# Kernel tuning notes

Measured on AMD Instinct MI355X. Metric: run time of the kernel, lower is better.

## Reference

```python
import jax, jax.numpy as jnp
import numpy as np

N_NODES = 20000
N_EDGES = 320000
HEADS = 16
NEG_SLOPE = 0.2


def _gat_conv(x, src, dst, W, a_src, a_dst, b, heads, out_ch):
    # x: [N, F_in]; src/dst: [E'] (self-loops already appended)
    N = x.shape[0]
    h = (x @ W).reshape(N, heads, out_ch)                  # [N, H, C]
    alpha_s = jnp.sum(h * a_src, axis=-1)                  # [N, H]
    alpha_d = jnp.sum(h * a_dst, axis=-1)                  # [N, H]
    e = jax.nn.leaky_relu(alpha_s[src] + alpha_d[dst], NEG_SLOPE)  # [E', H]
    # segment softmax over edges grouped by destination node
    m = jax.ops.segment_max(e, dst, num_segments=N)        # [N, H]
    ex = jnp.exp(e - m[dst])
    denom = jax.ops.segment_sum(ex, dst, num_segments=N)
    alpha = ex / (denom[dst] + 1e-16)                      # [E', H]
    msg = h[src] * alpha[:, :, None]                       # [E', H, C]
    out = jax.ops.segment_sum(msg, dst, num_segments=N)    # [N, H, C]
    return out.reshape(N, heads * out_ch) + b


def _forward(x, edge_index, params):
    N = x.shape[0]
    loops = jnp.arange(N, dtype=edge_index.dtype)
    src = jnp.concatenate([edge_index[0], loops])
    dst = jnp.concatenate([edge_index[1], loops])
    for i, (W, a_s, a_d, b, out_ch) in enumerate(params):
        x = _gat_conv(x, src, dst, W, a_s, a_d, b, HEADS, out_ch)
        if i < len(params) - 1:
            x = jax.nn.relu(x)
    return jnp.sum(x, axis=0, keepdims=True)               # [1, 768]


def setup_inputs() -> dict:
    key = jax.random.key(0)
    ks = jax.random.split(key, 32)
    hid, heads, out_c = 64, HEADS, 3
    dims = [(3, hid), (hid * heads, hid), (hid * heads, hid), (hid * heads, hid), (hid * heads, hid), (hid * heads, out_c * heads)]
    inp = {}
    inp["x"] = jax.random.normal(ks[0], (N_NODES, 3), dtype=jnp.float32)
    inp["edge_index"] = jax.random.randint(ks[1], (2, N_EDGES), 0, N_NODES, dtype=jnp.int64)
    k = 2
    for li, (fin, c) in enumerate(dims, start=1):
        inp[f"W{li}"] = jax.random.normal(ks[k], (fin, heads * c), dtype=jnp.float32) * 0.1; k += 1
        inp[f"a{li}s"] = jax.random.normal(ks[k], (heads, c), dtype=jnp.float32) * 0.1; k += 1
        inp[f"a{li}d"] = jax.random.normal(ks[k], (heads, c), dtype=jnp.float32) * 0.1; k += 1
        inp[f"b{li}"] = jnp.zeros((heads * c,), dtype=jnp.float32)
    return inp


def reference(x, edge_index, W1, a1s, a1d, b1, W2, a2s, a2d, b2, W3, a3s, a3d, b3, W4, a4s, a4d, b4, W5, a5s, a5d, b5, W6, a6s, a6d, b6):
    params = [
        (W1, a1s, a1d, b1, 64), (W2, a2s, a2d, b2, 64), (W3, a3s, a3d, b3, 64),
        (W4, a4s, a4d, b4, 64), (W5, a5s, a5d, b5, 64), (W6, a6s, a6d, b6, 48),
    ]
    return _forward(x, edge_index, params)
```

## Files before the change

### kernel.cpp

```cpp
#include <hip/hip_runtime.h>
#include <cstddef>
#include <cstdint>

#define N_NODES 20000
#define N_EDGES 320000
#define E_TOT   (N_EDGES + N_NODES)
#define HEADS   16
#define TILE_SHIFT 12
#define N_TILES 5

typedef __bf16 bf16;
typedef __attribute__((ext_vector_type(8))) __bf16 bf16x8;
typedef __attribute__((ext_vector_type(4))) __bf16 bf16x4;
typedef __attribute__((ext_vector_type(4))) float  f32x4;

__device__ __forceinline__ void gll16(const void* g, void* l) {
    __builtin_amdgcn_global_load_lds(
        (const __attribute__((address_space(1))) unsigned int*)g,
        (__attribute__((address_space(3))) unsigned int*)l, 16, 0, 0);
}

__global__ __launch_bounds__(256)
void k_lin1(const float* __restrict__ x, const float* __restrict__ W,
            const float* __restrict__ aS, const float* __restrict__ aD,
            bf16* __restrict__ hg, float* __restrict__ as_,
            float* __restrict__ ad_) {
    int n = blockIdx.x;
    int t = threadIdx.x;
    int f0 = t * 4, hd = t >> 4;
    float x0 = x[n*3+0], x1 = x[n*3+1], x2 = x[n*3+2];
    float v[4];
    bf16x4 hv;
#pragma unroll
    for (int c = 0; c < 4; ++c) {
        int f = f0 + c;
        v[c] = x0*W[f] + x1*W[1024+f] + x2*W[2048+f];
        hv[c] = (bf16)v[c];
    }
    *reinterpret_cast<bf16x4*>(&hg[(size_t)n * 1024 + f0]) = hv;
    float ps = 0.f, pd = 0.f;
    int cb = (t & 15) * 4;
#pragma unroll
    for (int c = 0; c < 4; ++c) {
        ps = fmaf(v[c], aS[hd*64 + cb + c], ps);
        pd = fmaf(v[c], aD[hd*64 + cb + c], pd);
    }
#pragma unroll
    for (int off = 1; off < 16; off <<= 1) {
        ps += __shfl_xor(ps, off);
        pd += __shfl_xor(pd, off);
    }
    if ((t & 15) == 0) {
        as_[n*16 + hd] = ps;
        ad_[n*16 + hd] = pd;
    }
}

__global__ __launch_bounds__(256)
void k_convW(const float* __restrict__ W, bf16* __restrict__ Th,
             bf16* __restrict__ Tl, int M) {
    __shared__ float t[32][33];
    int m0 = blockIdx.x * 32, k0 = blockIdx.y * 32;
    int j = threadIdx.x & 31, i0 = threadIdx.x >> 5;
#pragma unroll
    for (int s = 0; s < 4; ++s) {
        int i = i0 + s * 8;
        t[i][j] = W[(size_t)(k0 + i) * M + m0 + j];
    }
    __syncthreads();
#pragma unroll
    for (int s = 0; s < 4; ++s) {
        int i = i0 + s * 8;
        float v = t[j][i];
        bf16 hi = (bf16)v;
        Th[(size_t)(m0 + i) * 1024 + k0 + j] = hi;
        if (Tl) Tl[(size_t)(m0 + i) * 1024 + k0 + j] = (bf16)(v - (float)hi);
    }
}

template<bool FUSE, bool TWOB>
__global__ __launch_bounds__(256, 2)
void k_gemm3(const bf16* __restrict__ Ah,
             const bf16* __restrict__ Bh, const bf16* __restrict__ Bl,
             float* __restrict__ Cf, bf16* __restrict__ Ch,
             const float* __restrict__ aS, const float* __restrict__ aD,
             float* __restrict__ as_, float* __restrict__ ad_,
             int N, int M) {
    __shared__ __align__(16) bf16 sAh[128 * 32];
    __shared__ __align__(16) bf16 sBh[128 * 32];
    __shared__ __align__(16) bf16 sBl[TWOB ? 128 * 32 : 8];

    const int tid  = threadIdx.x;
    const int wid  = tid >> 6, lane = tid & 63;
    const int wr   = wid >> 1, wc = wid & 1;
    const int col0 = blockIdx.x * 128, row0 = blockIdx.y * 128;

    f32x4 acc[4][4] = {};

    const int rl = lane >> 2;
    const int gg = lane & 3;
    const int rb0 = wid * 32;
    const int lrow = lane & 15, g4 = lane >> 4;

    for (int k0 = 0; k0 < 1024; k0 += 32) {
#pragma unroll
        for (int half = 0; half < 2; ++half) {
            int rt = rb0 + half * 16 + rl;
            int kc = (gg ^ ((rt >> 1) & 3)) * 8;
            size_t lbase = (size_t)(rb0 + half * 16) * 32;
            int ar = row0 + rt; if (ar >= N) ar = N - 1;
            gll16(Ah + (size_t)ar * 1024 + k0 + kc, sAh + lbase);
            int br = col0 + rt;
            gll16(Bh + (size_t)br * 1024 + k0 + kc, sBh + lbase);
            if (TWOB) gll16(Bl + (size_t)br * 1024 + k0 + kc, sBl + lbase);
        }
        __syncthreads();

        bf16x8 ah[4], bh[4], bl[4];
#pragma unroll
        for (int m = 0; m < 4; ++m) {
            int r = wr * 64 + m * 16 + lrow;
            int off = r * 32 + ((g4 ^ ((r >> 1) & 3)) * 8);
            ah[m] = *(const bf16x8*)&sAh[off];
        }
#pragma unroll
        for (int n = 0; n < 4; ++n) {
            int r = wc * 64 + n * 16 + lrow;
            int off = r * 32 + ((g4 ^ ((r >> 1) & 3)) * 8);
            bh[n] = *(const bf16x8*)&sBh[off];
            if (TWOB) bl[n] = *(const bf16x8*)&sBl[off];
        }
#pragma unroll
        for (int m = 0; m < 4; ++m)
#pragma unroll
            for (int n = 0; n < 4; ++n) {
                acc[m][n] = __builtin_amdgcn_mfma_f32_16x16x32_bf16(ah[m], bh[n], acc[m][n], 0, 0, 0);
                if (TWOB)
                    acc[m][n] = __builtin_amdgcn_mfma_f32_16x16x32_bf16(ah[m], bl[n], acc[m][n], 0, 0, 0);
            }
        __syncthreads();
    }

    if (!FUSE) {
#pragma unroll
        for (int m = 0; m < 4; ++m) {
#pragma unroll
            for (int n = 0; n < 4; ++n) {
                int col = col0 + wc * 64 + n * 16 + lrow;
#pragma unroll
                for (int q = 0; q < 4; ++q) {
                    int row = row0 + wr * 64 + m * 16 + g4 * 4 + q;
                    if (row < N) {
                        float v = acc[m][n][q];
                        Cf[(size_t)row * M + col] = v;
                        Ch[(size_t)row * M + col] = (bf16)v;
                    }
                }
            }
        }
    }

    if (FUSE) {
        const int hd = blockIdx.x * 2 + wc;
        float asv[4], adv[4];
#pragma unroll
        for (int n = 0; n < 4; ++n) {
            asv[n] = aS[hd * 64 + n * 16 + lrow];
            adv[n] = aD[hd * 64 + n * 16 + lrow];
        }
        float ps[4][4], pd[4][4];
#pragma unroll
        for (int m = 0; m < 4; ++m)
#pragma unroll
            for (int q = 0; q < 4; ++q) {
                float s = 0.f, d = 0.f;
#pragma unroll
                for (int n = 0; n < 4; ++n) {
                    s = fmaf(acc[m][n][q], asv[n], s);
                    d = fmaf(acc[m][n][q], adv[n], d);
                }
                ps[m][q] = s; pd[m][q] = d;
            }
#pragma unroll
        for (int off = 1; off < 16; off <<= 1) {
#pragma unroll
            for (int m = 0; m < 4; ++m)
#pragma unroll
                for (int q = 0; q < 4; ++q) {
                    ps[m][q] += __shfl_xor(ps[m][q], off);
                    pd[m][q] += __shfl_xor(pd[m][q], off);
                }
        }
        if (lrow == 0) {
#pragma unroll
            for (int m = 0; m < 4; ++m)
#pragma unroll
                for (int q = 0; q < 4; ++q) {
                    int row = row0 + wr * 64 + m * 16 + g4 * 4 + q;
                    if (row < N) {
                        as_[row * 16 + hd] = ps[m][q];
                        ad_[row * 16 + hd] = pd[m][q];
                    }
                }
        }

        bf16* sC = sAh;
#pragma unroll
        for (int m = 0; m < 4; ++m) {
            __syncthreads();
#pragma unroll
            for (int n = 0; n < 4; ++n) {
#pragma unroll
                for (int q = 0; q < 4; ++q) {
                    int rh = wr * 16 + g4 * 4 + q;
                    int cc = wc * 64 + n * 16 + lrow;
                    sC[rh * 128 + cc] = (bf16)acc[m][n][q];
                }
            }
            __syncthreads();
#pragma unroll
            for (int it = 0; it < 2; ++it) {
                int rh = it * 16 + (tid >> 4);
                int cc = (tid & 15) * 8;
                int grow = row0 + (rh >> 4) * 64 + m * 16 + (rh & 15);
                if (grow < N) {
                    bf16x8 vv = *reinterpret_cast<const bf16x8*>(&sC[rh * 128 + cc]);
                    *reinterpret_cast<bf16x8*>(&Ch[(size_t)grow * M + col0 + cc]) = vv;
                }
            }
        }
    }
}

__global__ __launch_bounds__(256)
void k_alpha(const float* __restrict__ h, const float* __restrict__ a_s,
             const float* __restrict__ a_d, float* __restrict__ as_out,
             float* __restrict__ ad_out, int C, int M) {
    int pair = blockIdx.x * 4 + (threadIdx.x >> 6);
    int lane = threadIdx.x & 63;
    if (pair >= N_NODES * HEADS) return;
    int n = pair >> 4, hd = pair & 15;
    float vs = 0.f, vd = 0.f;
    if (lane < C) {
        float hv = h[(size_t)n * M + hd * C + lane];
        vs = hv * a_s[hd * C + lane];
        vd = hv * a_d[hd * C + lane];
    }
#pragma unroll
    for (int off = 32; off > 0; off >>= 1) {
        vs += __shfl_down(vs, off);
        vd += __shfl_down(vd, off);
    }
    if (lane == 0) { as_out[pair] = vs; ad_out[pair] = vd; }
}

__global__ void k_zero_i(int* __restrict__ p, int n) {
    int t = blockIdx.x * 256 + threadIdx.x;
    if (t < n) p[t] = 0;
}
__global__ void k_hist(const int* __restrict__ ei, int* __restrict__ deg) {
    int e = blockIdx.x * 256 + threadIdx.x;
    if (e >= E_TOT) return;
    int d = (e < N_EDGES) ? ei[N_EDGES + e] : e - N_EDGES;
    atomicAdd(&deg[d], 1);
}
__global__ __launch_bounds__(256)
void k_scan(const int* __restrict__ deg, int* __restrict__ rowstart,
            int* __restrict__ cursor) {
    __shared__ int sh[256];
    int carry = 0;
    for (int base = 0; base < N_NODES; base += 256) {
        int i = base + threadIdx.x;
        int v = (i < N_NODES) ? deg[i] : 0;
        sh[threadIdx.x] = v;
        __syncthreads();
        for (int off = 1; off < 256; off <<= 1) {
            int t = (threadIdx.x >= off) ? sh[threadIdx.x - off] : 0;
            __syncthreads();
            sh[threadIdx.x] += t;
            __syncthreads();
        }
        if (i < N_NODES) {
            int excl = carry + sh[threadIdx.x] - v;
            rowstart[i] = excl;
            cursor[i] = excl;
        }
        carry += sh[255];
        __syncthreads();
    }
    if (threadIdx.x == 0) rowstart[N_NODES] = carry;
}
__global__ void k_scatter(const int* __restrict__ ei, int* __restrict__ cursor,
                          int* __restrict__ csr_src) {
    int e = blockIdx.x * 256 + threadIdx.x;
    if (e >= E_TOT) return;
    int s, d;
    if (e < N_EDGES) { s = ei[e]; d = ei[N_EDGES + e]; }
    else             { s = d = e - N_EDGES; }
    int slot = atomicAdd(&cursor[d], 1);
    csr_src[slot] = s;
}

__global__ __launch_bounds__(256)
void k_rowsort(const int* __restrict__ rowstart, const int* __restrict__ csr_src,
               int* __restrict__ csr_src2, int* __restrict__ csr_dst2) {
    int n = blockIdx.x * 256 + threadIdx.x;
    if (n >= N_NODES) return;
    int s0 = rowstart[n], s1 = rowstart[n + 1];
    int cnt[N_TILES];
#pragma unroll
    for (int t = 0; t < N_TILES; ++t) cnt[t] = 0;
    for (int j = s0; j < s1; ++j) cnt[csr_src[j] >> TILE_SHIFT]++;
    int off[N_TILES];
    int acc = s0;
#pragma unroll
    for (int t = 0; t < N_TILES; ++t) { off[t] = acc; acc += cnt[t]; }
    for (int j = s0; j < s1; ++j) {
        int s = csr_src[j];
        int slot = off[s >> TILE_SHIFT]++;
        csr_src2[slot] = s;
        csr_dst2[slot] = n;
    }
}

__global__ __launch_bounds__(256)
void k_mden(const int* __restrict__ rowstart, const int* __restrict__ csr_src,
            const float* __restrict__ as_, const float* __restrict__ ad_,
            float* __restrict__ m_, float* __restrict__ inv_) {
    int n = blockIdx.x * 4 + (threadIdx.x >> 6);
    int lane = threadIdx.x & 63;
    int hd = lane & 15;
    int strip = lane >> 4;
    int s0 = rowstart[n], s1 = rowstart[n + 1];
    float adv = ad_[n * 16 + hd];
    float m = -1e30f, den = 0.f;
    for (int j = s0 + strip; j < s1; j += 4) {
        float v = as_[csr_src[j] * 16 + hd] + adv;
        v = v > 0.f ? v : 0.2f * v;
        float nm = fmaxf(m, v);
        float rm = __expf(m - nm);
        float re = __expf(v - nm);
        den = den * rm + re;
        m = nm;
    }
#pragma unroll
    for (int off = 16; off <= 32; off <<= 1) {
        float mo = __shfl_xor(m, off);
        float dn = __shfl_xor(den, off);
        float nm = fmaxf(m, mo);
        den = den * __expf(m - nm) + dn * __expf(mo - nm);
        m = nm;
    }
    if (strip == 0) {
        m_[n * 16 + hd] = m;
        inv_[n * 16 + hd] = 1.f / (den + 1e-16f);
    }
}

__global__ __launch_bounds__(256)
void k_alpha_w(const int* __restrict__ csr_src, const int* __restrict__ csr_dst,
               const float* __restrict__ as_, const float* __restrict__ ad_,
               const float* __restrict__ m_, const float* __restrict__ inv_,
               float* __restrict__ alpha) {
    int t = blockIdx.x * 256 + threadIdx.x;
    if (t >= E_TOT * HEADS) return;
    int j = t >> 4, hd = t & 15;
    int s = csr_src[j], d = csr_dst[j];
    float v = as_[s * 16 + hd] + ad_[d * 16 + hd];
    v = v > 0.f ? v : 0.2f * v;
    alpha[t] = __expf(v - m_[d * 16 + hd]) * inv_[d * 16 + hd];
}

__global__ __launch_bounds__(256)
void k_agg1024(const bf16* __restrict__ hg, const int* __restrict__ rowstart,
               const int* __restrict__ csr_src, const float* __restrict__ alpha,
               const float* __restrict__ bias, bf16* __restrict__ oh) {
    int n = blockIdx.y * 16 + (threadIdx.x >> 4);
    int sub = threadIdx.x & 15;
    int f0 = blockIdx.x * 128 + sub * 8;
    int hd = f0 >> 6;
    int s0 = rowstart[n], s1 = rowstart[n + 1];
    float acc[8] = {};
#pragma unroll 2
    for (int j = s0; j < s1; ++j) {
        int s = csr_src[j];
        float a = alpha[(size_t)j * 16 + hd];
        bf16x8 hv = *reinterpret_cast<const bf16x8*>(&hg[(size_t)s * 1024 + f0]);
#pragma unroll
        for (int c = 0; c < 8; ++c)
            acc[c] = fmaf(a, (float)hv[c], acc[c]);
    }
    bf16x8 vh;
#pragma unroll
    for (int c = 0; c < 8; ++c) {
        float r = fmaxf(acc[c] + bias[f0 + c], 0.f);
        vh[c] = (bf16)r;
    }
    *reinterpret_cast<bf16x8*>(&oh[(size_t)n * 1024 + f0]) = vh;
}

__global__ __launch_bounds__(256)
void k_agg768(const bf16* __restrict__ hg, const int* __restrict__ rowstart,
              const int* __restrict__ csr_src, const float* __restrict__ alpha,
              const float* __restrict__ bias, float* __restrict__ out) {
    int n = blockIdx.x * 2 + (threadIdx.x >> 7);
    int tloc = threadIdx.x & 127;
    if (tloc >= 96) return;
    int f0 = tloc * 8;
    int hd = f0 / 48;
    int s0 = rowstart[n], s1 = rowstart[n + 1];
    float acc[8] = {};
#pragma unroll 2
    for (int j = s0; j < s1; ++j) {
        int s = csr_src[j];
        float a = alpha[(size_t)j * 16 + hd];
        bf16x8 hv = *reinterpret_cast<const bf16x8*>(&hg[(size_t)s * 768 + f0]);
#pragma unroll
        for (int c = 0; c < 8; ++c)
            acc[c] = fmaf(a, (float)hv[c], acc[c]);
    }
#pragma unroll
    for (int c = 0; c < 8; ++c)
        out[(size_t)n * 768 + f0 + c] = acc[c] + bias[f0 + c];
}

__global__ __launch_bounds__(256)
void k_colsum(const float* __restrict__ x, float* __restrict__ out) {
    int f = blockIdx.x * 256 + threadIdx.x;
    int chunk = blockIdx.y;
    int n0 = chunk * 625, n1 = n0 + 625;
    float s = 0.f;
    for (int n = n0; n < n1; ++n) s += x[(size_t)n * 768 + f];
    atomicAdd(&out[f], s);
}

extern "C" void kernel_launch(void* const* d_in, const int* in_sizes, int n_in,
                              void* d_out, int out_size, void* d_ws, size_t ws_size,
                              hipStream_t stream) {
    const float* x0 = (const float*)d_in[0];
    const int*   ei = (const int*)d_in[1];

    char* w = (char*)d_ws;
    float* xB  = (float*)w;
    float* xOut = (float*)w;
    w += (size_t)N_NODES * 1024 * sizeof(float);
    bf16*  hgat = (bf16*)w; w += (size_t)N_NODES * 1024 * sizeof(bf16);
    bf16*  x_hi = (bf16*)w; w += (size_t)N_NODES * 1024 * sizeof(bf16);
    float* as_  = (float*)w; w += (size_t)N_NODES * HEADS * sizeof(float);
    float* ad_  = (float*)w; w += (size_t)N_NODES * HEADS * sizeof(float);
    float* m_   = (float*)w; w += (size_t)N_NODES * HEADS * sizeof(float);
    float* inv_ = (float*)w; w += (size_t)N_NODES * HEADS * sizeof(float);
    float* alpha = (float*)w; w += (size_t)E_TOT * HEADS * sizeof(float);
    bf16* Wt_hi = (bf16*)w; w += (size_t)1024 * 1024 * sizeof(bf16);
    bf16* Wt_lo = (bf16*)w; w += (size_t)1024 * 1024 * sizeof(bf16);
    int* deg      = (int*)w; w += N_NODES * sizeof(int);
    int* rowstart = (int*)w; w += (N_NODES + 1) * sizeof(int);
    int* cursor   = (int*)w; w += N_NODES * sizeof(int);
    int* csr_src  = (int*)w; w += E_TOT * sizeof(int);
    int* csr_src2 = (int*)w; w += E_TOT * sizeof(int);
    int* csr_dst2 = (int*)w; w += E_TOT * sizeof(int);

    k_zero_i<<<(N_NODES + 255) / 256, 256, 0, stream>>>(deg, N_NODES);
    k_hist<<<(E_TOT + 255) / 256, 256, 0, stream>>>(ei, deg);
    k_scan<<<1, 256, 0, stream>>>(deg, rowstart, cursor);
    k_scatter<<<(E_TOT + 255) / 256, 256, 0, stream>>>(ei, cursor, csr_src);
    k_rowsort<<<(N_NODES + 255) / 256, 256, 0, stream>>>(rowstart, csr_src, csr_src2, csr_dst2);

    for (int l = 0; l < 6; ++l) {
        const float* W  = (const float*)d_in[2 + 4 * l + 0];
        const float* aS = (const float*)d_in[2 + 4 * l + 1];
        const float* aD = (const float*)d_in[2 + 4 * l + 2];
        const float* bv = (const float*)d_in[2 + 4 * l + 3];
        int M = (l == 5) ? 768 : 1024;

        if (l == 0) {
            k_lin1<<<N_NODES, 256, 0, stream>>>(x0, W, aS, aD, hgat, as_, ad_);
        } else {
            dim3 tg(M / 32, 32);
            dim3 grid(M / 128, (N_NODES + 127) / 128);
            if (l < 5) {
                k_convW<<<tg, 256, 0, stream>>>(W, Wt_hi, nullptr, M);
                k_gemm3<true, false><<<grid, 256, 0, stream>>>(
                    x_hi, Wt_hi, nullptr, nullptr, hgat, aS, aD, as_, ad_,
                    N_NODES, M);
            } else {
                k_convW<<<tg, 256, 0, stream>>>(W, Wt_hi, Wt_lo, M);
                k_gemm3<false, true><<<grid, 256, 0, stream>>>(
                    x_hi, Wt_hi, Wt_lo, xB, hgat, nullptr, nullptr,
                    nullptr, nullptr, N_NODES, M);
                k_alpha<<<(N_NODES * HEADS + 3) / 4, 256, 0, stream>>>(
                    xB, aS, aD, as_, ad_, 48, 768);
            }
        }
        k_mden<<<N_NODES / 4, 256, 0, stream>>>(rowstart, csr_src2, as_, ad_, m_, inv_);
        k_alpha_w<<<(E_TOT * HEADS + 255) / 256, 256, 0, stream>>>(
            csr_src2, csr_dst2, as_, ad_, m_, inv_, alpha);
        if (l < 5) {
            dim3 agrid(8, N_NODES / 16);
            k_agg1024<<<agrid, 256, 0, stream>>>(
                hgat, rowstart, csr_src2, alpha, bv, x_hi);
        } else {
            k_agg768<<<N_NODES / 2, 256, 0, stream>>>(
                hgat, rowstart, csr_src2, alpha, bv, xOut);
        }
    }

    hipMemsetAsync(d_out, 0, (size_t)out_size * sizeof(float), stream);
    dim3 cgrid(3, 32);
    k_colsum<<<cgrid, 256, 0, stream>>>(xOut, (float*)d_out);
}
```

Measured before the change: 1.274 ms.

## Double-buffer LDS tiles in bf16 GEMM to overlap global loads with MFMA

The GEMM now keeps two LDS buffers for the A, B and B-low tiles. It issues the async global-to-LDS loads for the next K step before computing on the current one, with one barrier per iteration instead of two. The aim is to hide global load latency behind MFMA work. LDS use doubles, which may reduce occupancy under launch_bounds(256,2). Correctness depends on the single barrier being enough to cover completion of the async loads.

```diff
diff --git a/kernel.cpp b/kernel.cpp
--- a/kernel.cpp
+++ b/kernel.cpp
@@ -86,9 +86,9 @@
              const float* __restrict__ aS, const float* __restrict__ aD,
              float* __restrict__ as_, float* __restrict__ ad_,
              int N, int M) {
-    __shared__ __align__(16) bf16 sAh[128 * 32];
-    __shared__ __align__(16) bf16 sBh[128 * 32];
-    __shared__ __align__(16) bf16 sBl[TWOB ? 128 * 32 : 8];
+    __shared__ __align__(16) bf16 sA[2][128 * 32];
+    __shared__ __align__(16) bf16 sB[2][128 * 32];
+    __shared__ __align__(16) bf16 sL[TWOB ? 2 : 1][TWOB ? 128 * 32 : 8];
 
     const int tid  = threadIdx.x;
     const int wid  = tid >> 6, lane = tid & 63;
@@ -102,33 +102,43 @@
     const int rb0 = wid * 32;
     const int lrow = lane & 15, g4 = lane >> 4;
 
-    for (int k0 = 0; k0 < 1024; k0 += 32) {
-#pragma unroll
-        for (int half = 0; half < 2; ++half) {
-            int rt = rb0 + half * 16 + rl;
-            int kc = (gg ^ ((rt >> 1) & 3)) * 8;
-            size_t lbase = (size_t)(rb0 + half * 16) * 32;
-            int ar = row0 + rt; if (ar >= N) ar = N - 1;
-            gll16(Ah + (size_t)ar * 1024 + k0 + kc, sAh + lbase);
-            int br = col0 + rt;
-            gll16(Bh + (size_t)br * 1024 + k0 + kc, sBh + lbase);
-            if (TWOB) gll16(Bl + (size_t)br * 1024 + k0 + kc, sBl + lbase);
-        }
-        __syncthreads();
+    int rt0 = rb0 + rl, rt1 = rb0 + 16 + rl;
+    int kc0 = (gg ^ ((rt0 >> 1) & 3)) * 8;
+    int kc1 = (gg ^ ((rt1 >> 1) & 3)) * 8;
+    size_t lb0 = (size_t)rt0 * 32, lb1 = (size_t)rt1 * 32;
+    int ar0 = row0 + rt0; if (ar0 >= N) ar0 = N - 1;
+    int ar1 = row0 + rt1; if (ar1 >= N) ar1 = N - 1;
+    int br0 = col0 + rt0, br1 = col0 + rt1;
+
+    auto STAGE = [&](int buf, int k0) {
+        gll16(Ah + (size_t)ar0 * 1024 + k0 + kc0, &sA[buf][lb0]);
+        gll16(Bh + (size_t)br0 * 1024 + k0 + kc0, &sB[buf][lb0]);
+        if (TWOB) gll16(Bl + (size_t)br0 * 1024 + k0 + kc0, &sL[buf][lb0]);
+        gll16(Ah + (size_t)ar1 * 1024 + k0 + kc1, &sA[buf][lb1]);
+        gll16(Bh + (size_t)br1 * 1024 + k0 + kc1, &sB[buf][lb1]);
+        if (TWOB) gll16(Bl + (size_t)br1 * 1024 + k0 + kc1, &sL[buf][lb1]);
+    };
+
+    STAGE(0, 0);
+    __syncthreads();
+
+    int cur = 0;
+    for (int t = 0; t < 32; ++t) {
+        if (t + 1 < 32) STAGE(cur ^ 1, (t + 1) * 32);
 
         bf16x8 ah[4], bh[4], bl[4];
 #pragma unroll
         for (int m = 0; m < 4; ++m) {
             int r = wr * 64 + m * 16 + lrow;
             int off = r * 32 + ((g4 ^ ((r >> 1) & 3)) * 8);
-            ah[m] = *(const bf16x8*)&sAh[off];
+            ah[m] = *(const bf16x8*)&sA[cur][off];
         }
 #pragma unroll
         for (int n = 0; n < 4; ++n) {
             int r = wc * 64 + n * 16 + lrow;
             int off = r * 32 + ((g4 ^ ((r >> 1) & 3)) * 8);
-            bh[n] = *(const bf16x8*)&sBh[off];
-            if (TWOB) bl[n] = *(const bf16x8*)&sBl[off];
+            bh[n] = *(const bf16x8*)&sB[cur][off];
+            if (TWOB) bl[n] = *(const bf16x8*)&sL[cur][off];
         }
 #pragma unroll
         for (int m = 0; m < 4; ++m)
@@ -139,6 +149,7 @@
                     acc[m][n] = __builtin_amdgcn_mfma_f32_16x16x32_bf16(ah[m], bl[n], acc[m][n], 0, 0, 0);
             }
         __syncthreads();
+        cur ^= 1;
     }
 
     if (!FUSE) {
@@ -204,7 +215,7 @@
                 }
         }
 
-        bf16* sC = sAh;
+        bf16* sC = &sA[0][0];
 #pragma unroll
         for (int m = 0; m < 4; ++m) {
             __syncthreads();
```

Result: no change. 1.273 ms (-0.1%).
